# Kernel tuning notes

Measured on AMD Instinct MI355X. Metric: run time of the kernel, lower is better.

## Reference

```python
import jax, jax.numpy as jnp
import numpy as np
import math

H, DK, DV = 16, 64, 64
D = H * DK  # model_dimension = 1024
N = M = L = 2048


def setup_inputs() -> dict:
    key = jax.random.key(0)
    ks = jax.random.split(key, 12)
    s = 1.0 / math.sqrt(DK)  # keep softmax logits in a sane range
    return {
        "queries": jax.random.normal(ks[0], (N, DK), jnp.float32),
        "keys": jax.random.normal(ks[1], (M, DK), jnp.float32),
        "values": jax.random.normal(ks[2], (L, DV), jnp.float32),
        "Wq": jax.random.normal(ks[3], (H, DK, D), jnp.float32) * s,
        "bq": jax.random.normal(ks[4], (H, D), jnp.float32) * 0.02,
        "Wk": jax.random.normal(ks[5], (H, DK, D), jnp.float32) * s,
        "bk": jax.random.normal(ks[6], (H, D), jnp.float32) * 0.02,
        "Wv": jax.random.normal(ks[7], (H, DV, D), jnp.float32) * s,
        "bv": jax.random.normal(ks[8], (H, D), jnp.float32) * 0.02,
        "Wo": jax.random.normal(ks[9], (D, H * DV), jnp.float32) * (1.0 / math.sqrt(H * DV)),
        "bo": jax.random.normal(ks[10], (D,), jnp.float32) * 0.02,
    }


def reference(queries, keys, values, Wq, bq, Wk, bk, Wv, bv, Wo, bo):
    # Batched per-head projections (original loops over heads in Python).
    Qp = jnp.einsum("nk,hkd->hnd", queries, Wq) + bq[:, None, :]   # (H, N, D)
    Kp = jnp.einsum("mk,hkd->hmd", keys, Wk) + bk[:, None, :]      # (H, M, D)
    Vp = jnp.einsum("lv,hvd->hld", values, Wv) + bv[:, None, :]    # (H, M, D)
    scores = jnp.einsum("hnd,hmd->hnm", Qp, Kp) / math.sqrt(DK)
    attn = jax.nn.softmax(scores, axis=-1)
    heads_out = jnp.einsum("hnm,hmd->hnd", attn, Vp)               # (H, N, D)
    # torch.concat(heads, dim=0).sum(dim=0) == sum over heads AND rows -> (D,)
    pooled = heads_out.sum(axis=(0, 1)).reshape(1, D)
    return pooled @ Wo.T + bo  # (1, D)
```

## Files before the change

kernel.cpp:

```cpp
#include <hip/hip_runtime.h>


typedef __attribute__((ext_vector_type(4))) float floatx4;
typedef __attribute__((ext_vector_type(8))) short shortx8;

__device__ inline unsigned short f2bf(float f) {
    unsigned int u = __float_as_uint(f);
    u += 0x7FFFu + ((u >> 16) & 1u);
    return (unsigned short)(u >> 16);
}
__device__ inline float bf2f(unsigned short s) {
    return __uint_as_float(((unsigned int)s) << 16);
}

#define SWZ(row, bc) ((row) * 128 + ((bc) ^ (((row) & 7) << 4)))
#define QSCALE 0.18033688f

__global__ __launch_bounds__(256) void prep_kernel(
    const float* __restrict__ Wq, const float* __restrict__ Wk,
    const float* __restrict__ bq, const float* __restrict__ keys,
    float* __restrict__ Apart, float* __restrict__ vhpart,
    unsigned short* __restrict__ Kb, float* __restrict__ r_ws) {
    const int tid = threadIdx.x;
    const int bx = blockIdx.x;
    __shared__ __align__(16) unsigned char sm[36352];
    if (bx < 128) {
        const int g = bx >> 4, h = bx & 15;
        const int c0 = g * 128;
        unsigned short* wq = (unsigned short*)sm;
        unsigned short* wk = (unsigned short*)(sm + 17408);
        float* bqs = (float*)(sm + 34816);
        float* vred = (float*)(sm + 35328);
        {
            int row = tid >> 2, cs = (tid & 3) * 32;
            const float* wqp = Wq + (size_t)(h * 64 + row) * 1024 + c0 + cs;
            const float* wkp = Wk + (size_t)(h * 64 + row) * 1024 + c0 + cs;
            #pragma unroll
            for (int u = 0; u < 8; ++u) {
                float4 a = *(const float4*)&wqp[u * 4];
                float4 b = *(const float4*)&wkp[u * 4];
                *(ushort4*)&wq[row * 136 + cs + u * 4] =
                    (ushort4){f2bf(a.x), f2bf(a.y), f2bf(a.z), f2bf(a.w)};
                *(ushort4*)&wk[row * 136 + cs + u * 4] =
                    (ushort4){f2bf(b.x), f2bf(b.y), f2bf(b.z), f2bf(b.w)};
            }
            if (tid < 128) bqs[tid] = bq[h * 1024 + c0 + tid];
        }
        __syncthreads();
        const int w = tid >> 6, lane = tid & 63;
        const int ln = lane & 15, quad = lane >> 4;
        {
            const int j = tid & 63, half = tid >> 6;
            float accv = 0.f;
            #pragma unroll
            for (int u = 0; u < 32; ++u)
                accv += bf2f(wk[j * 136 + half * 32 + u]) * bqs[half * 32 + u];
            vred[half * 64 + j] = accv;
        }
        shortx8 af[4];
        #pragma unroll
        for (int kk = 0; kk < 4; ++kk)
            af[kk] = *(shortx8*)&wq[(w * 16 + ln) * 136 + kk * 32 + quad * 8];
        float* ap = Apart + (size_t)bx * 4096;
        #pragma unroll
        for (int cn = 0; cn < 4; ++cn) {
            floatx4 acc = {};
            #pragma unroll
            for (int kk = 0; kk < 4; ++kk) {
                shortx8 bf_ = *(shortx8*)&wk[(cn * 16 + ln) * 136 + kk * 32 + quad * 8];
                acc = __builtin_amdgcn_mfma_f32_16x16x32_bf16(af[kk], bf_, acc, 0, 0, 0);
            }
            #pragma unroll
            for (int r = 0; r < 4; ++r)
                ap[(w * 16 + quad * 4 + r) * 64 + cn * 16 + ln] = acc[r];
        }
        __syncthreads();
        if (tid < 64)
            vhpart[bx * 64 + tid] = vred[tid] + vred[64 + tid] +
                                    vred[128 + tid] + vred[192 + tid];
    } else {
        int bk = bx - 128;
        int base = (bk * 256 + tid) * 32;
        #pragma unroll
        for (int u = 0; u < 8; ++u) {
            float4 a = *(const float4*)&keys[base + u * 4];
            *(ushort4*)&Kb[base + u * 4] =
                (ushort4){f2bf(a.x), f2bf(a.y), f2bf(a.z), f2bf(a.w)};
        }
        if (tid < 64) r_ws[bk * 64 + tid] = 0.f;
    }
}

__global__ __launch_bounds__(256) void reduceA_kernel(
    const float* __restrict__ Apart, const float* __restrict__ vhpart,
    unsigned short* __restrict__ Atlg, float* __restrict__ vhg) {
    const int tid = threadIdx.x;
    const int h = blockIdx.x >> 2, uq = blockIdx.x & 3;
    #pragma unroll
    for (int uu = 0; uu < 4; ++uu) {
        int e = (uq * 4 + uu) * 256 + tid;
        float s = 0.f;
        #pragma unroll
        for (int g = 0; g < 8; ++g)
            s += Apart[g * 65536 + h * 4096 + e];
        Atlg[h * 4096 + (e & 63) * 64 + (e >> 6)] = f2bf(s);
    }
    if (uq == 0 && tid < 64) {
        float s = 0.f;
        #pragma unroll
        for (int g = 0; g < 8; ++g) s += vhpart[(g * 16 + h) * 64 + tid];
        vhg[h * 64 + tid] = s;
    }
}

__global__ __launch_bounds__(256, 4) void pass1_kernel(
    const float* __restrict__ queries, const unsigned short* __restrict__ Atlg,
    const float* __restrict__ vhg, const unsigned short* __restrict__ Kb,
    unsigned short* __restrict__ Qhs, float* __restrict__ u_ws) {
    const int h = blockIdx.y;
    const int n0 = blockIdx.x * 64;
    const int tid = threadIdx.x;
    const int w = tid >> 6, lane = tid & 63;
    const int ln = lane & 15, quad = lane >> 4;

    __shared__ __align__(16) unsigned char lds[27648];
    __shared__ float vhs[64];
    unsigned short* qstage = (unsigned short*)lds;
    unsigned short* Atl = (unsigned short*)(lds + 9216);
    unsigned short* qh = (unsigned short*)(lds + 18432);

    {
        int row = tid >> 2, c16 = (tid & 3) * 16;
        const float* qp = queries + (size_t)(n0 + row) * 64 + c16;
        #pragma unroll
        for (int u = 0; u < 4; ++u) {
            float4 a = *(const float4*)&qp[u * 4];
            *(ushort4*)&qstage[row * 72 + c16 + u * 4] =
                (ushort4){f2bf(a.x), f2bf(a.y), f2bf(a.z), f2bf(a.w)};
        }
        #pragma unroll
        for (int u = 0; u < 2; ++u)
            *(shortx8*)&Atl[row * 72 + c16 + u * 8] =
                *(const shortx8*)&Atlg[h * 4096 + row * 64 + c16 + u * 8];
    }
    if (tid < 64) vhs[tid] = vhg[h * 64 + tid];
    __syncthreads();

    {
        shortx8 qa[2];
        #pragma unroll
        for (int kk = 0; kk < 2; ++kk)
            qa[kk] = *(shortx8*)&qstage[(w * 16 + ln) * 72 + kk * 32 + quad * 8];
        #pragma unroll
        for (int cn = 0; cn < 4; ++cn) {
            floatx4 acc = {};
            #pragma unroll
            for (int kk = 0; kk < 2; ++kk) {
                shortx8 bfr = *(shortx8*)&Atl[(cn * 16 + ln) * 72 + kk * 32 + quad * 8];
                acc = __builtin_amdgcn_mfma_f32_16x16x32_bf16(qa[kk], bfr, acc, 0, 0, 0);
            }
            #pragma unroll
            for (int r = 0; r < 4; ++r)
                qh[(w * 16 + quad * 4 + r) * 72 + cn * 16 + ln] =
                    f2bf((acc[r] + vhs[cn * 16 + ln]) * QSCALE);
        }
    }
    __syncthreads();

    #pragma unroll
    for (int k = 0; k < 2; ++k) {
        int seg = tid * 2 + k, row = seg >> 3, off = (seg & 7) * 8;
        *(shortx8*)&Qhs[((size_t)h * 2048 + n0 + row) * 64 + off] =
            *(shortx8*)&qh[row * 72 + off];
    }
    const int srow = tid >> 2, sc = (tid & 3) * 16;
    #pragma unroll
    for (int i = 0; i < 2; ++i)
        *(shortx8*)(lds + SWZ(srow, sc * 2 + i * 16)) =
            *(const shortx8*)&Kb[(size_t)srow * 64 + sc + i * 8];
    shortx8 qf[2];
    #pragma unroll
    for (int kk = 0; kk < 2; ++kk)
        qf[kk] = *(shortx8*)&qh[(w * 16 + ln) * 72 + kk * 32 + quad * 8];
    __syncthreads();

    float lacc[4] = {};
    for (int s = 0; s < 32; ++s) {
        const unsigned char* kb = lds + (s & 1) * 8192;
        shortx8 krn[2];
        if (s < 31) {
            int m0n = (s + 1) * 64;
            #pragma unroll
            for (int i = 0; i < 2; ++i)
                krn[i] = *(const shortx8*)&Kb[(size_t)(m0n + srow) * 64 + sc + i * 8];
        }
        #pragma unroll
        for (int cm = 0; cm < 4; ++cm) {
            shortx8 kf0 = *(const shortx8*)(kb + SWZ(cm * 16 + ln, quad * 16));
            shortx8 kf1 = *(const shortx8*)(kb + SWZ(cm * 16 + ln, 64 + quad * 16));
            floatx4 acc = {};
            acc = __builtin_amdgcn_mfma_f32_16x16x32_bf16(qf[0], kf0, acc, 0, 0, 0);
            acc = __builtin_amdgcn_mfma_f32_16x16x32_bf16(qf[1], kf1, acc, 0, 0, 0);
            #pragma unroll
            for (int r = 0; r < 4; ++r)
                lacc[r] += __builtin_amdgcn_exp2f(acc[r]);
        }
        if (s < 31) {
            unsigned char* kbn = lds + (((s & 1) ^ 1)) * 8192;
            #pragma unroll
            for (int i = 0; i < 2; ++i)
                *(shortx8*)(kbn + SWZ(srow, sc * 2 + i * 16)) = krn[i];
        }
        __syncthreads();
    }

    #pragma unroll
    for (int r = 0; r < 4; ++r) {
        float x = lacc[r];
        #pragma unroll
        for (int o = 1; o <= 8; o <<= 1) x += __shfl_xor(x, o);
        if (ln == 0)
            u_ws[(size_t)h * 2048 + n0 + w * 16 + quad * 4 + r] = 1.0f / x;
    }
}

__global__ __launch_bounds__(256, 4) void pass2_kernel(
    const unsigned short* __restrict__ Qhs, const float* __restrict__ u_ws,
    const unsigned short* __restrict__ Kb, const float* __restrict__ values,
    float* __restrict__ r_ws) {
    const int h = blockIdx.y;
    const int mb = blockIdx.x * 64;
    const int tid = threadIdx.x;
    const int w = tid >> 6, lane = tid & 63;
    const int ln = lane & 15, quad = lane >> 4;

    __shared__ __align__(16) unsigned char lds[18176];
    float* u_sb = (float*)(lds + 16384);
    float* g_s = (float*)(lds + 16896);
    float* Rred = (float*)(lds + 17152);

    shortx8 kf[2];
    #pragma unroll
    for (int kk = 0; kk < 2; ++kk)
        kf[kk] = *(const shortx8*)&Kb[(size_t)(mb + w * 16 + ln) * 64 + kk * 32 + quad * 8];

    const int srow = tid >> 2, sc = (tid & 3) * 16;
    #pragma unroll
    for (int i = 0; i < 2; ++i)
        *(shortx8*)(lds + SWZ(srow, sc * 2 + i * 16)) =
            *(const shortx8*)&Qhs[((size_t)h * 2048 + srow) * 64 + sc + i * 8];
    if (tid < 64) u_sb[tid] = u_ws[(size_t)h * 2048 + tid];
    __syncthreads();

    float gacc = 0.f;
    for (int s = 0; s < 32; ++s) {
        const unsigned char* qb = lds + (s & 1) * 8192;
        const float* us = u_sb + (s & 1) * 64;
        shortx8 qrn[2];
        float urn = 0.f;
        if (s < 31) {
            int n0n = (s + 1) * 64;
            #pragma unroll
            for (int i = 0; i < 2; ++i)
                qrn[i] = *(const shortx8*)&Qhs[((size_t)h * 2048 + n0n + srow) * 64 + sc + i * 8];
            if (tid < 64) urn = u_ws[(size_t)h * 2048 + n0n + tid];
        }
        #pragma unroll
        for (int rt = 0; rt < 4; ++rt) {
            shortx8 qa0 = *(const shortx8*)(qb + SWZ(rt * 16 + ln, quad * 16));
            shortx8 qa1 = *(const shortx8*)(qb + SWZ(rt * 16 + ln, 64 + quad * 16));
            floatx4 acc = {};
            acc = __builtin_amdgcn_mfma_f32_16x16x32_bf16(qa0, kf[0], acc, 0, 0, 0);
            acc = __builtin_amdgcn_mfma_f32_16x16x32_bf16(qa1, kf[1], acc, 0, 0, 0);
            #pragma unroll
            for (int r = 0; r < 4; ++r)
                gacc += __builtin_amdgcn_exp2f(acc[r]) * us[rt * 16 + quad * 4 + r];
        }
        if (s < 31) {
            unsigned char* qbn = lds + (((s & 1) ^ 1)) * 8192;
            #pragma unroll
            for (int i = 0; i < 2; ++i)
                *(shortx8*)(qbn + SWZ(srow, sc * 2 + i * 16)) = qrn[i];
            if (tid < 64) u_sb[((s & 1) ^ 1) * 64 + tid] = urn;
        }
        __syncthreads();
    }

    gacc += __shfl_xor(gacc, 16);
    gacc += __shfl_xor(gacc, 32);
    if (quad == 0) g_s[w * 16 + ln] = gacc;
    __syncthreads();
    {
        int grp = tid >> 6, v = tid & 63;
        float acc = 0.f;
        #pragma unroll
        for (int j = 0; j < 16; ++j)
            acc += g_s[grp * 16 + j] *
                   values[(size_t)(mb + grp * 16 + j) * 64 + v];
        Rred[grp * 64 + v] = acc;
    }
    __syncthreads();
    if (tid < 64)
        atomicAdd(&r_ws[h * 64 + tid],
                  Rred[tid] + Rred[64 + tid] + Rred[128 + tid] + Rred[192 + tid]);
}

__global__ __launch_bounds__(256) void pool_kernel(
    const float* __restrict__ Wv, const float* __restrict__ bv,
    const float* __restrict__ r_ws, float* __restrict__ pooled) {
    const int tid = threadIdx.x;
    const int d0 = blockIdx.x * 16;
    const int d = tid & 15, hh = tid >> 4;
    __shared__ float red[16][17];
    float acc = bv[hh * 1024 + d0 + d] * 2048.0f;
    const float* rv = r_ws + hh * 64;
    const float* wp = Wv + (size_t)hh * 64 * 1024 + d0 + d;
    #pragma unroll 8
    for (int v = 0; v < 64; ++v) acc += rv[v] * wp[(size_t)v * 1024];
    red[hh][d] = acc;
    __syncthreads();
    if (tid < 16) {
        float s = 0.f;
        #pragma unroll
        for (int g = 0; g < 16; ++g) s += red[g][tid];
        pooled[d0 + tid] = s;
    }
}

__global__ __launch_bounds__(256) void out_kernel(
    const float* __restrict__ Wo, const float* __restrict__ bo,
    const float* __restrict__ pooled, float* __restrict__ out) {
    const int tid = threadIdx.x, w = tid >> 6, lane = tid & 63;
    const int dp = blockIdx.x * 4 + w;
    const float* wr = Wo + (size_t)dp * 1024 + lane * 16;
    const float* pp = pooled + lane * 16;
    float acc = 0.f;
    #pragma unroll
    for (int u = 0; u < 4; ++u) {
        float4 a = *(const float4*)&wr[u * 4];
        float4 p = *(const float4*)&pp[u * 4];
        acc += a.x * p.x + a.y * p.y + a.z * p.z + a.w * p.w;
    }
    #pragma unroll
    for (int o = 32; o > 0; o >>= 1) acc += __shfl_xor(acc, o);
    if (lane == 0) out[dp] = acc + bo[dp];
}

extern "C" void kernel_launch(void* const* d_in, const int* in_sizes, int n_in,
                              void* d_out, int out_size, void* d_ws, size_t ws_size,
                              hipStream_t stream) {
    const float* queries = (const float*)d_in[0];
    const float* keys    = (const float*)d_in[1];
    const float* values  = (const float*)d_in[2];
    const float* Wq      = (const float*)d_in[3];
    const float* bq      = (const float*)d_in[4];
    const float* Wk      = (const float*)d_in[5];
    const float* Wv      = (const float*)d_in[7];
    const float* bv      = (const float*)d_in[8];
    const float* Wo      = (const float*)d_in[9];
    const float* bo      = (const float*)d_in[10];
    float* out = (float*)d_out;

    char* base = (char*)d_ws;
    unsigned short* Qhs = (unsigned short*)base;
    float* Apart  = (float*)base;
    float* vhpart = Apart + 524288;
    float* u_ws   = (float*)(base + 4194304);
    float* r_ws   = (float*)(base + 4325376);
    float* pooled = (float*)(base + 4329472);
    unsigned short* Kb   = (unsigned short*)(base + 4333568);
    unsigned short* Atlg = (unsigned short*)(base + 4595712);
    float* vhg    = (float*)(base + 4726784);

    prep_kernel<<<144, 256, 0, stream>>>(Wq, Wk, bq, keys,
                                         Apart, vhpart, Kb, r_ws);
    reduceA_kernel<<<64, 256, 0, stream>>>(Apart, vhpart, Atlg, vhg);
    pass1_kernel<<<dim3(32, 16), 256, 0, stream>>>(queries, Atlg, vhg,
                                                   Kb, Qhs, u_ws);
    pass2_kernel<<<dim3(32, 16), 256, 0, stream>>>(Qhs, u_ws, Kb, values, r_ws);
    pool_kernel<<<64, 256, 0, stream>>>(Wv, bv, r_ws, pooled);
    out_kernel<<<256, 256, 0, stream>>>(Wo, bo, pooled, out);
}
```

Measured before the change: 137.7 us.

## Fuse A reduction into prep and split pass1/pass2 across two halves

The prep kernel now has one block per head loop over all eight column groups, accumulating the Wq·Wk^T product in registers. That removes the Apart partial buffer and the separate reduceA kernel launch, but leaves only 16 blocks doing the heavy prep work. Pass1 and pass2 each double their grid by splitting the key range (pass1) or query range (pass2) in half. Pass1 now combines the partial softmax denominators with atomicAdd into a zeroed l_ws buffer, and pass2 takes reciprocals on load. The aim is better occupancy on the main passes and one fewer launch, at the cost of a serialized prep and atomic traffic.

Measured after the change: 199.4 us. +44.9%, slower.

```diff
diff --git a/kernel.cpp b/kernel.cpp
--- a/kernel.cpp
+++ b/kernel.cpp
@@ -19,67 +19,78 @@
 __global__ __launch_bounds__(256) void prep_kernel(
     const float* __restrict__ Wq, const float* __restrict__ Wk,
     const float* __restrict__ bq, const float* __restrict__ keys,
-    float* __restrict__ Apart, float* __restrict__ vhpart,
-    unsigned short* __restrict__ Kb, float* __restrict__ r_ws) {
+    unsigned short* __restrict__ Atlg, float* __restrict__ vhg,
+    unsigned short* __restrict__ Kb, float* __restrict__ l_ws,
+    float* __restrict__ r_ws) {
     const int tid = threadIdx.x;
     const int bx = blockIdx.x;
     __shared__ __align__(16) unsigned char sm[36352];
-    if (bx < 128) {
-        const int g = bx >> 4, h = bx & 15;
-        const int c0 = g * 128;
+    if (bx < 16) {
+        const int h = bx;
         unsigned short* wq = (unsigned short*)sm;
         unsigned short* wk = (unsigned short*)(sm + 17408);
         float* bqs = (float*)(sm + 34816);
         float* vred = (float*)(sm + 35328);
-        {
-            int row = tid >> 2, cs = (tid & 3) * 32;
-            const float* wqp = Wq + (size_t)(h * 64 + row) * 1024 + c0 + cs;
-            const float* wkp = Wk + (size_t)(h * 64 + row) * 1024 + c0 + cs;
-            #pragma unroll
-            for (int u = 0; u < 8; ++u) {
-                float4 a = *(const float4*)&wqp[u * 4];
-                float4 b = *(const float4*)&wkp[u * 4];
-                *(ushort4*)&wq[row * 136 + cs + u * 4] =
-                    (ushort4){f2bf(a.x), f2bf(a.y), f2bf(a.z), f2bf(a.w)};
-                *(ushort4*)&wk[row * 136 + cs + u * 4] =
-                    (ushort4){f2bf(b.x), f2bf(b.y), f2bf(b.z), f2bf(b.w)};
-            }
-            if (tid < 128) bqs[tid] = bq[h * 1024 + c0 + tid];
-        }
-        __syncthreads();
         const int w = tid >> 6, lane = tid & 63;
         const int ln = lane & 15, quad = lane >> 4;
-        {
-            const int j = tid & 63, half = tid >> 6;
-            float accv = 0.f;
-            #pragma unroll
-            for (int u = 0; u < 32; ++u)
-                accv += bf2f(wk[j * 136 + half * 32 + u]) * bqs[half * 32 + u];
-            vred[half * 64 + j] = accv;
-        }
-        shortx8 af[4];
-        #pragma unroll
-        for (int kk = 0; kk < 4; ++kk)
-            af[kk] = *(shortx8*)&wq[(w * 16 + ln) * 136 + kk * 32 + quad * 8];
-        float* ap = Apart + (size_t)bx * 4096;
-        #pragma unroll
-        for (int cn = 0; cn < 4; ++cn) {
-            floatx4 acc = {};
-            #pragma unroll
-            for (int kk = 0; kk < 4; ++kk) {
-                shortx8 bf_ = *(shortx8*)&wk[(cn * 16 + ln) * 136 + kk * 32 + quad * 8];
-                acc = __builtin_amdgcn_mfma_f32_16x16x32_bf16(af[kk], bf_, acc, 0, 0, 0);
+        floatx4 acc[4] = {};
+        float vreg = 0.f;
+        for (int g = 0; g < 8; ++g) {
+            const int c0 = g * 128;
+            {
+                int row = tid >> 2, cs = (tid & 3) * 32;
+                const float* wqp = Wq + (size_t)(h * 64 + row) * 1024 + c0 + cs;
+                const float* wkp = Wk + (size_t)(h * 64 + row) * 1024 + c0 + cs;
+                #pragma unroll
+                for (int u = 0; u < 8; ++u) {
+                    float4 a = *(const float4*)&wqp[u * 4];
+                    float4 b = *(const float4*)&wkp[u * 4];
+                    *(ushort4*)&wq[row * 136 + cs + u * 4] =
+                        (ushort4){f2bf(a.x), f2bf(a.y), f2bf(a.z), f2bf(a.w)};
+                    *(ushort4*)&wk[row * 136 + cs + u * 4] =
+                        (ushort4){f2bf(b.x), f2bf(b.y), f2bf(b.z), f2bf(b.w)};
+                }
+                if (tid < 128) bqs[tid] = bq[h * 1024 + c0 + tid];
             }
+            __syncthreads();
+            {
+                const int j = tid & 63, half = tid >> 6;
+                #pragma unroll
+                for (int u = 0; u < 32; ++u)
+                    vreg += bf2f(wk[j * 136 + half * 32 + u]) * bqs[half * 32 + u];
+            }
+            shortx8 af[4];
+            #pragma unroll
+            for (int kk = 0; kk < 4; ++kk)
+                af[kk] = *(shortx8*)&wq[(w * 16 + ln) * 136 + kk * 32 + quad * 8];
+            #pragma unroll
+            for (int cn = 0; cn < 4; ++cn)
+                #pragma unroll
+                for (int kk = 0; kk < 4; ++kk) {
+                    shortx8 bf_ = *(shortx8*)&wk[(cn * 16 + ln) * 136 + kk * 32 + quad * 8];
+                    acc[cn] = __builtin_amdgcn_mfma_f32_16x16x32_bf16(af[kk], bf_, acc[cn], 0, 0, 0);
+                }
+            __syncthreads();
+        }
+        vred[(tid >> 6) * 64 + (tid & 63)] = vreg;
+        unsigned short* atl = (unsigned short*)sm;
+        #pragma unroll
+        for (int cn = 0; cn < 4; ++cn)
             #pragma unroll
             for (int r = 0; r < 4; ++r)
-                ap[(w * 16 + quad * 4 + r) * 64 + cn * 16 + ln] = acc[r];
-        }
+                atl[(cn * 16 + ln) * 72 + w * 16 + quad * 4 + r] = f2bf(acc[cn][r]);
         __syncthreads();
+        #pragma unroll
+        for (int k = 0; k < 2; ++k) {
+            int seg = tid * 2 + k, row = seg >> 3, off = (seg & 7) * 8;
+            *(shortx8*)&Atlg[h * 4096 + row * 64 + off] =
+                *(shortx8*)&atl[row * 72 + off];
+        }
         if (tid < 64)
-            vhpart[bx * 64 + tid] = vred[tid] + vred[64 + tid] +
-                                    vred[128 + tid] + vred[192 + tid];
+            vhg[h * 64 + tid] = vred[tid] + vred[64 + tid] +
+                                vred[128 + tid] + vred[192 + tid];
     } else {
-        int bk = bx - 128;
+        int bk = bx - 16;
         int base = (bk * 256 + tid) * 32;
         #pragma unroll
         for (int u = 0; u < 8; ++u) {
@@ -87,38 +98,19 @@
             *(ushort4*)&Kb[base + u * 4] =
                 (ushort4){f2bf(a.x), f2bf(a.y), f2bf(a.z), f2bf(a.w)};
         }
+        #pragma unroll
+        for (int i = 0; i < 8; ++i) l_ws[bk * 2048 + tid * 8 + i] = 0.f;
         if (tid < 64) r_ws[bk * 64 + tid] = 0.f;
-    }
-}
-
-__global__ __launch_bounds__(256) void reduceA_kernel(
-    const float* __restrict__ Apart, const float* __restrict__ vhpart,
-    unsigned short* __restrict__ Atlg, float* __restrict__ vhg) {
-    const int tid = threadIdx.x;
-    const int h = blockIdx.x >> 2, uq = blockIdx.x & 3;
-    #pragma unroll
-    for (int uu = 0; uu < 4; ++uu) {
-        int e = (uq * 4 + uu) * 256 + tid;
-        float s = 0.f;
-        #pragma unroll
-        for (int g = 0; g < 8; ++g)
-            s += Apart[g * 65536 + h * 4096 + e];
-        Atlg[h * 4096 + (e & 63) * 64 + (e >> 6)] = f2bf(s);
-    }
-    if (uq == 0 && tid < 64) {
-        float s = 0.f;
-        #pragma unroll
-        for (int g = 0; g < 8; ++g) s += vhpart[(g * 16 + h) * 64 + tid];
-        vhg[h * 64 + tid] = s;
     }
 }
 
 __global__ __launch_bounds__(256, 4) void pass1_kernel(
     const float* __restrict__ queries, const unsigned short* __restrict__ Atlg,
     const float* __restrict__ vhg, const unsigned short* __restrict__ Kb,
-    unsigned short* __restrict__ Qhs, float* __restrict__ u_ws) {
+    unsigned short* __restrict__ Qhs, float* __restrict__ l_ws) {
     const int h = blockIdx.y;
-    const int n0 = blockIdx.x * 64;
+    const int nt = blockIdx.x >> 1, kh = blockIdx.x & 1;
+    const int n0 = nt * 64;
     const int tid = threadIdx.x;
     const int w = tid >> 6, lane = tid & 63;
     const int ln = lane & 15, quad = lane >> 4;
@@ -167,17 +159,20 @@
     }
     __syncthreads();
 
-    #pragma unroll
-    for (int k = 0; k < 2; ++k) {
-        int seg = tid * 2 + k, row = seg >> 3, off = (seg & 7) * 8;
-        *(shortx8*)&Qhs[((size_t)h * 2048 + n0 + row) * 64 + off] =
-            *(shortx8*)&qh[row * 72 + off];
-    }
+    if (kh == 0) {
+        #pragma unroll
+        for (int k = 0; k < 2; ++k) {
+            int seg = tid * 2 + k, row = seg >> 3, off = (seg & 7) * 8;
+            *(shortx8*)&Qhs[((size_t)h * 2048 + n0 + row) * 64 + off] =
+                *(shortx8*)&qh[row * 72 + off];
+        }
+    }
+    const int mbase = kh * 1024;
     const int srow = tid >> 2, sc = (tid & 3) * 16;
     #pragma unroll
     for (int i = 0; i < 2; ++i)
         *(shortx8*)(lds + SWZ(srow, sc * 2 + i * 16)) =
-            *(const shortx8*)&Kb[(size_t)srow * 64 + sc + i * 8];
+            *(const shortx8*)&Kb[(size_t)(mbase + srow) * 64 + sc + i * 8];
     shortx8 qf[2];
     #pragma unroll
     for (int kk = 0; kk < 2; ++kk)
@@ -185,11 +180,11 @@
     __syncthreads();
 
     float lacc[4] = {};
-    for (int s = 0; s < 32; ++s) {
+    for (int s = 0; s < 16; ++s) {
         const unsigned char* kb = lds + (s & 1) * 8192;
         shortx8 krn[2];
-        if (s < 31) {
-            int m0n = (s + 1) * 64;
+        if (s < 15) {
+            int m0n = mbase + (s + 1) * 64;
             #pragma unroll
             for (int i = 0; i < 2; ++i)
                 krn[i] = *(const shortx8*)&Kb[(size_t)(m0n + srow) * 64 + sc + i * 8];
@@ -205,7 +200,7 @@
             for (int r = 0; r < 4; ++r)
                 lacc[r] += __builtin_amdgcn_exp2f(acc[r]);
         }
-        if (s < 31) {
+        if (s < 15) {
             unsigned char* kbn = lds + (((s & 1) ^ 1)) * 8192;
             #pragma unroll
             for (int i = 0; i < 2; ++i)
@@ -220,16 +215,18 @@
         #pragma unroll
         for (int o = 1; o <= 8; o <<= 1) x += __shfl_xor(x, o);
         if (ln == 0)
-            u_ws[(size_t)h * 2048 + n0 + w * 16 + quad * 4 + r] = 1.0f / x;
+            atomicAdd(&l_ws[(size_t)h * 2048 + n0 + w * 16 + quad * 4 + r], x);
     }
 }
 
 __global__ __launch_bounds__(256, 4) void pass2_kernel(
-    const unsigned short* __restrict__ Qhs, const float* __restrict__ u_ws,
+    const unsigned short* __restrict__ Qhs, const float* __restrict__ l_ws,
     const unsigned short* __restrict__ Kb, const float* __restrict__ values,
     float* __restrict__ r_ws) {
     const int h = blockIdx.y;
-    const int mb = blockIdx.x * 64;
+    const int mt = blockIdx.x >> 1, nh = blockIdx.x & 1;
+    const int mb = mt * 64;
+    const int nbase = nh * 1024;
     const int tid = threadIdx.x;
     const int w = tid >> 6, lane = tid & 63;
     const int ln = lane & 15, quad = lane >> 4;
@@ -248,22 +245,22 @@
     #pragma unroll
     for (int i = 0; i < 2; ++i)
         *(shortx8*)(lds + SWZ(srow, sc * 2 + i * 16)) =
-            *(const shortx8*)&Qhs[((size_t)h * 2048 + srow) * 64 + sc + i * 8];
-    if (tid < 64) u_sb[tid] = u_ws[(size_t)h * 2048 + tid];
+            *(const shortx8*)&Qhs[((size_t)h * 2048 + nbase + srow) * 64 + sc + i * 8];
+    if (tid < 64) u_sb[tid] = 1.0f / l_ws[(size_t)h * 2048 + nbase + tid];
     __syncthreads();
 
     float gacc = 0.f;
-    for (int s = 0; s < 32; ++s) {
+    for (int s = 0; s < 16; ++s) {
         const unsigned char* qb = lds + (s & 1) * 8192;
         const float* us = u_sb + (s & 1) * 64;
         shortx8 qrn[2];
         float urn = 0.f;
-        if (s < 31) {
-            int n0n = (s + 1) * 64;
+        if (s < 15) {
+            int n0n = nbase + (s + 1) * 64;
             #pragma unroll
             for (int i = 0; i < 2; ++i)
                 qrn[i] = *(const shortx8*)&Qhs[((size_t)h * 2048 + n0n + srow) * 64 + sc + i * 8];
-            if (tid < 64) urn = u_ws[(size_t)h * 2048 + n0n + tid];
+            if (tid < 64) urn = 1.0f / l_ws[(size_t)h * 2048 + n0n + tid];
         }
         #pragma unroll
         for (int rt = 0; rt < 4; ++rt) {
@@ -276,7 +273,7 @@
             for (int r = 0; r < 4; ++r)
                 gacc += __builtin_amdgcn_exp2f(acc[r]) * us[rt * 16 + quad * 4 + r];
         }
-        if (s < 31) {
+        if (s < 15) {
             unsigned char* qbn = lds + (((s & 1) ^ 1)) * 8192;
             #pragma unroll
             for (int i = 0; i < 2; ++i)
@@ -363,21 +360,18 @@
 
     char* base = (char*)d_ws;
     unsigned short* Qhs = (unsigned short*)base;
-    float* Apart  = (float*)base;
-    float* vhpart = Apart + 524288;
-    float* u_ws   = (float*)(base + 4194304);
+    float* l_ws   = (float*)(base + 4194304);
     float* r_ws   = (float*)(base + 4325376);
     float* pooled = (float*)(base + 4329472);
     unsigned short* Kb   = (unsigned short*)(base + 4333568);
     unsigned short* Atlg = (unsigned short*)(base + 4595712);
     float* vhg    = (float*)(base + 4726784);
 
-    prep_kernel<<<144, 256, 0, stream>>>(Wq, Wk, bq, keys,
-                                         Apart, vhpart, Kb, r_ws);
-    reduceA_kernel<<<64, 256, 0, stream>>>(Apart, vhpart, Atlg, vhg);
-    pass1_kernel<<<dim3(32, 16), 256, 0, stream>>>(queries, Atlg, vhg,
-                                                   Kb, Qhs, u_ws);
-    pass2_kernel<<<dim3(32, 16), 256, 0, stream>>>(Qhs, u_ws, Kb, values, r_ws);
+    prep_kernel<<<32, 256, 0, stream>>>(Wq, Wk, bq, keys,
+                                        Atlg, vhg, Kb, l_ws, r_ws);
+    pass1_kernel<<<dim3(64, 16), 256, 0, stream>>>(queries, Atlg, vhg,
+                                                   Kb, Qhs, l_ws);
+    pass2_kernel<<<dim3(64, 16), 256, 0, stream>>>(Qhs, l_ws, Kb, values, r_ws);
     pool_kernel<<<64, 256, 0, stream>>>(Wv, bv, r_ws, pooled);
     out_kernel<<<256, 256, 0, stream>>>(Wo, bo, pooled, out);
 }
```
